# Performance work log

Hardware: AMD Instinct MI355X
Metric: run time of the kernel (lower is better)

The kernel has to match this reference:

```python
import jax, jax.numpy as jnp
import numpy as np

BN_EPS = 1e-3  # keras BatchNormalization default epsilon
B, T, D, V = 2048, 100, 64, 200000
N_OTHER, V_OTHER, D_OTHER = 2, 10000, 32
DNN = (256, 128, 64)


def _gru(seq_x, Wx, Wh, b, valid, att=None):
    """GRU / AUGRU scan. seq_x [B,T,D]; valid [B,T] bool; att [B,T] or None.
    AUGRU: update gate z is scaled by the attention score a_t;
    invalid (padded) steps hold the previous state (dynamic length)."""
    Bs, Ts, _ = seq_x.shape
    H = Wh.shape[0]
    xproj = jnp.einsum('btd,dh->bth', seq_x, Wx) + b          # [B,T,3H]
    xproj = jnp.transpose(xproj, (1, 0, 2))                    # [T,B,3H]
    v = jnp.transpose(valid, (1, 0))[:, :, None]               # [T,B,1]
    if att is None:
        a = jnp.ones((Ts, Bs, 1), seq_x.dtype)
    else:
        a = jnp.transpose(att, (1, 0))[:, :, None]
    h0 = jnp.zeros((Bs, H), seq_x.dtype)

    def step(h, inp):
        xp, vi, ai = inp
        xz, xr, xh = jnp.split(xp, 3, -1)
        hz, hr, hh = jnp.split(h @ Wh, 3, -1)
        z = jax.nn.sigmoid(xz + hz) * ai
        r = jax.nn.sigmoid(xr + hr)
        cand = jnp.tanh(xh + r * hh)
        hn = (1.0 - z) * h + z * cand
        hn = jnp.where(vi, hn, h)
        return hn, hn

    final, seq = jax.lax.scan(step, h0, (xproj, v, a))
    return final, jnp.transpose(seq, (1, 0, 2))                # [B,T,H]


def _dice(x, alpha):
    # Dice activation, inference-mode BN (moving mean 0, var 1)
    p = jax.nn.sigmoid(x * (1.0 / np.sqrt(1.0 + BN_EPS)))
    return p * x + (1.0 - p) * alpha * x


def _attention(q, keys, mask, W1, b1, W2, b2, W3, b3):
    # DIN-style attention: MLP over [q, k, q-k, q*k], masked softmax over time
    qe = jnp.broadcast_to(q[:, None, :], keys.shape)
    info = jnp.concatenate([qe, keys, qe - keys, qe * keys], -1)   # [B,T,4D]
    h = jax.nn.sigmoid(info @ W1 + b1)
    h = jax.nn.sigmoid(h @ W2 + b2)
    logits = (h @ W3 + b3)[..., 0]                                  # [B,T]
    logits = jnp.where(mask, logits, jnp.float32(-1e9))
    return jax.nn.softmax(logits, axis=-1)


def setup_inputs() -> dict:
    key = jax.random.key(0)
    ks = jax.random.split(key, 32)
    s = 0.05
    inp = {
        'dense_inputs': jax.random.normal(ks[0], (B, 8), jnp.float32),
        'sparse_inputs': jax.random.randint(ks[1], (B, N_OTHER), 0, V_OTHER, jnp.int32),
        'seq_inputs': jax.random.randint(ks[2], (B, T, 1), 0, V, jnp.int32),
        'no_click_seq': jax.random.randint(ks[3], (B, T, 1), 0, V, jnp.int32),
        'item_inputs': jax.random.randint(ks[4], (B, 1), 0, V, jnp.int32),
        'hist_real_len': jax.random.randint(ks[5], (B,), 1, T + 1, jnp.int32),
        'emb_item': jax.random.normal(ks[6], (V, D), jnp.float32) * s,
        'emb_neg': jax.random.normal(ks[7], (V, D), jnp.float32) * s,
        'emb_other': jax.random.normal(ks[8], (N_OTHER, V_OTHER, D_OTHER), jnp.float32) * s,
        'gru1_Wx': jax.random.normal(ks[9], (D, 3 * D), jnp.float32) * s,
        'gru1_Wh': jax.random.normal(ks[10], (D, 3 * D), jnp.float32) * s,
        'gru1_b': jnp.zeros((3 * D,), jnp.float32),
        'att_W1': jax.random.normal(ks[11], (4 * D, 64), jnp.float32) * s,
        'att_b1': jnp.zeros((64,), jnp.float32),
        'att_W2': jax.random.normal(ks[12], (64, 16), jnp.float32) * s,
        'att_b2': jnp.zeros((16,), jnp.float32),
        'att_W3': jax.random.normal(ks[13], (16, 1), jnp.float32) * s,
        'att_b3': jnp.zeros((1,), jnp.float32),
        'gru2_Wx': jax.random.normal(ks[14], (D, 3 * D), jnp.float32) * s,
        'gru2_Wh': jax.random.normal(ks[15], (D, 3 * D), jnp.float32) * s,
        'gru2_b': jnp.zeros((3 * D,), jnp.float32),
    }
    in_dim = D + D + 8 + N_OTHER * D_OTHER  # final_state + target + other_info
    inp['bn_gamma'] = jnp.ones((in_dim,), jnp.float32)
    inp['bn_beta'] = jnp.zeros((in_dim,), jnp.float32)
    dims = (in_dim,) + DNN
    for i in range(3):
        inp[f'ffn_W{i}'] = jax.random.normal(ks[16 + i], (dims[i], dims[i + 1]), jnp.float32) * s
        inp[f'ffn_b{i}'] = jnp.zeros((dims[i + 1],), jnp.float32)
        inp[f'dice_a{i}'] = jnp.full((dims[i + 1],), 0.25, jnp.float32)
    inp['out_W'] = jax.random.normal(ks[20], (DNN[-1], 1), jnp.float32) * s
    inp['out_b'] = jnp.zeros((1,), jnp.float32)
    return inp


def reference(dense_inputs, sparse_inputs, seq_inputs, no_click_seq, item_inputs,
              hist_real_len, emb_item, emb_neg, emb_other, gru1_Wx, gru1_Wh, gru1_b,
              att_W1, att_b1, att_W2, att_b2, att_W3, att_b3, gru2_Wx, gru2_Wh, gru2_b,
              bn_gamma, bn_beta, ffn_W0, ffn_b0, dice_a0, ffn_W1, ffn_b1, dice_a1,
              ffn_W2, ffn_b2, dice_a2, out_W, out_b):
    # other (non-behavior) info: dense feats ++ other sparse embeddings
    other = jnp.concatenate(
        [dense_inputs] + [emb_other[i][sparse_inputs[:, i]] for i in range(N_OTHER)], -1)
    seq_embed = emb_item[seq_inputs[:, :, 0]]          # [B,T,D]
    neg_embed = emb_neg[no_click_seq[:, :, 0]]         # [B,T,D]
    target = emb_item[item_inputs[:, 0]]               # [B,D]
    mask = seq_inputs[:, :, 0] != 0                    # [B,T]
    valid = jnp.arange(T)[None, :] < hist_real_len[:, None]

    # interest extraction: plain GRU over behavior sequence
    _, seq_h = _gru(seq_embed, gru1_Wx, gru1_Wh, gru1_b, valid)

    # auxiliary loss: h_t should predict the next clicked item vs a negative
    m = mask[:, 1:].astype(seq_h.dtype)
    h = seq_h[:, :-1]
    p_pos = jax.nn.sigmoid(jnp.sum(h * seq_embed[:, 1:], -1))
    p_neg = jax.nn.sigmoid(jnp.sum(h * neg_embed[:, 1:], -1))
    aux_loss = -jnp.sum(m * (jnp.log(p_pos + 1e-8) + jnp.log(1.0 - p_neg + 1e-8))) / (jnp.sum(m) + 1e-8)

    # interest evolution: attention-gated AUGRU
    scores = _attention(target, seq_h, mask, att_W1, att_b1, att_W2, att_b2, att_W3, att_b3)
    final_state, _ = _gru(seq_h, gru2_Wx, gru2_Wh, gru2_b, valid, att=scores)

    x = jnp.concatenate([final_state, target, other], -1)
    x = bn_gamma * x * (1.0 / np.sqrt(1.0 + BN_EPS)) + bn_beta   # inference BN
    x = _dice(x @ ffn_W0 + ffn_b0, dice_a0)
    x = _dice(x @ ffn_W1 + ffn_b1, dice_a1)
    x = _dice(x @ ffn_W2 + ffn_b2, dice_a2)
    out = jax.nn.sigmoid(x @ out_W + out_b)                       # [B,1]
    return out, aux_loss
```

## Files before the change

kernel.cpp:

```cpp
#include <hip/hip_runtime.h>
#include <math.h>


#define DEV __device__ __forceinline__

constexpr int BB = 2048;
constexpr int TT = 100;

typedef __attribute__((ext_vector_type(8))) short bf16x8;
typedef __attribute__((ext_vector_type(4))) float f32x4;

#define MFMA16(a, b, c) __builtin_amdgcn_mfma_f32_16x16x32_bf16(a, b, c, 0, 0, 0)

DEV float sigmoidf_(float x) { return 1.0f / (1.0f + __expf(-x)); }
DEV float tanhf_(float x)    { return 1.0f - 2.0f / (__expf(2.0f * x) + 1.0f); }
DEV short f2bf(float f) {
    unsigned u = __float_as_uint(f);
    u = (u + 0x7FFFu + ((u >> 16) & 1u)) >> 16;
    return (short)u;
}
DEV float bf2f(short s) { return __uint_as_float(((unsigned)(unsigned short)s) << 16); }

DEV void sync_lds() {
    __builtin_amdgcn_sched_barrier(0);
    asm volatile("s_waitcnt lgkmcnt(0)\n\ts_barrier" ::: "memory");
    __builtin_amdgcn_sched_barrier(0);
}

__global__ void k_prep(const float* __restrict__ W1, float* Wq, float* Wk, float* Wp, float* aux_acc) {
    int i = blockIdx.x * 256 + threadIdx.x;
    if (i < 4096) {
        int k = i >> 6, c = i & 63;
        float a  = W1[k * 64 + c];
        float bb = W1[(64 + k) * 64 + c];
        float cc = W1[(128 + k) * 64 + c];
        float dd = W1[(192 + k) * 64 + c];
        Wq[i] = a + cc;
        Wk[i] = bb - cc;
        Wp[i] = dd;
    }
    if (blockIdx.x == 0 && threadIdx.x == 0) { aux_acc[0] = 0.0f; aux_acc[1] = 0.0f; }
}

__global__ __launch_bounds__(256)
void k_prepW(const float* __restrict__ Wa, const float* __restrict__ Wb,
             const float* __restrict__ Wc, const float* __restrict__ Wd,
             short* __restrict__ oa, short* __restrict__ ob,
             short* __restrict__ oc, short* __restrict__ od) {
    const float* W; short* o;
    switch (blockIdx.y) {
        case 0:  W = Wa; o = oa; break;
        case 1:  W = Wb; o = ob; break;
        case 2:  W = Wc; o = oc; break;
        default: W = Wd; o = od; break;
    }
    int d = blockIdx.x * 256 + threadIdx.x;
    int frag = d >> 9, l = (d >> 3) & 63, i = d & 7;
    int n = frag >> 1, kt = frag & 1;
    int k = kt * 32 + ((l >> 4) << 3) + i;
    int c = (n << 4) + (l & 15);
    o[d] = f2bf(W[k * 192 + c]);
}

__global__ __launch_bounds__(256)
void k_prepA(const float* __restrict__ Wk, const float* __restrict__ Wp,
             short* __restrict__ oK, short* __restrict__ oP) {
    int d = blockIdx.x * 256 + threadIdx.x;
    int mat = d >> 12, i = d & 4095;
    int f = i >> 9, l = (i >> 3) & 63, e = i & 7;
    int kt = f >> 2, n = f & 3;
    int k = kt * 32 + ((l >> 4) << 3) + e;
    int c = (n << 4) + (l & 15);
    if (mat == 0) oK[i] = f2bf(Wk[k * 64 + c]);
    else          oP[i] = f2bf(Wp[k * 64 + c]);
}

__global__ __launch_bounds__(64)
void k_target(const int* __restrict__ item, const float* __restrict__ emb_item,
              const float* __restrict__ Wq, const float* __restrict__ b1,
              float* target, float* qproj) {
    int b = blockIdx.x, c = threadIdx.x;
    __shared__ float q[64];
    int idx = item[b];
    float tv = emb_item[(size_t)idx * 64 + c];
    target[b * 64 + c] = tv;
    q[c] = tv;
    __syncthreads();
    float acc = b1[c];
#pragma unroll
    for (int k = 0; k < 64; ++k) acc = fmaf(q[k], Wq[k * 64 + c], acc);
    qproj[b * 64 + c] = acc;
}

template <int MODE>
__global__ __launch_bounds__(256, 2)
void k_scan(const int* __restrict__ seq_idx, const float* __restrict__ embf,
            const short* __restrict__ seqb,
            const short* __restrict__ WxB, const short* __restrict__ WhB,
            const float* __restrict__ bias, const int* __restrict__ hist_len,
            const float* __restrict__ scores,
            short* __restrict__ seq_out, float* __restrict__ final_out) {
    __shared__ short hA[2][1024];

    const int tid  = threadIdx.x;
    const int w    = tid >> 6;
    const int lane = tid & 63;
    const int lr   = lane & 15;
    const int kg   = lane >> 4;
    const int b0   = blockIdx.x * 4;

    for (int i = tid; i < 2048; i += 256) ((short*)hA)[i] = 0;

    bf16x8 bx[3][2], bh[3][2];
#pragma unroll
    for (int n3 = 0; n3 < 3; ++n3) {
        int n = w + n3 * 4;
#pragma unroll
        for (int kt = 0; kt < 2; ++kt) {
            bx[n3][kt] = *(const bf16x8*)(WxB + (((n * 2 + kt) * 64 + lane) << 3));
            bh[n3][kt] = *(const bf16x8*)(WhB + (((n * 2 + kt) * 64 + lane) << 3));
        }
    }

    const int   c0  = (w << 4) + lr;
    const float bz  = bias[c0];
    const float brr = bias[64 + c0];
    const float bhb = bias[128 + c0];
    const bool  act = (kg == 0);

    int   hist[4];
    float h[4] = {0.f, 0.f, 0.f, 0.f};
#pragma unroll
    for (int j = 0; j < 4; ++j) hist[j] = hist_len[b0 + j];

    const int rload = (lr < 4) ? lr : 3;
    bf16x8 ecb0, ecb1;
    float  scc[4] = {1.f, 1.f, 1.f, 1.f};

    {
        if (MODE == 0) {
            int idx = seq_idx[(b0 + rload) * TT];
            const float* eb = embf + (size_t)idx * 64;
            float4 f0 = *(const float4*)(eb + kg * 8);
            float4 f1 = *(const float4*)(eb + kg * 8 + 4);
            float4 f2 = *(const float4*)(eb + 32 + kg * 8);
            float4 f3 = *(const float4*)(eb + 32 + kg * 8 + 4);
            ecb0[0] = f2bf(f0.x); ecb0[1] = f2bf(f0.y); ecb0[2] = f2bf(f0.z); ecb0[3] = f2bf(f0.w);
            ecb0[4] = f2bf(f1.x); ecb0[5] = f2bf(f1.y); ecb0[6] = f2bf(f1.z); ecb0[7] = f2bf(f1.w);
            ecb1[0] = f2bf(f2.x); ecb1[1] = f2bf(f2.y); ecb1[2] = f2bf(f2.z); ecb1[3] = f2bf(f2.w);
            ecb1[4] = f2bf(f3.x); ecb1[5] = f2bf(f3.y); ecb1[6] = f2bf(f3.z); ecb1[7] = f2bf(f3.w);
        } else {
            const short* eb = seqb + ((size_t)(b0 + rload) * TT) * 64;
            ecb0 = *(const bf16x8*)(eb + kg * 8);
            ecb1 = *(const bf16x8*)(eb + 32 + kg * 8);
        }
        if (MODE == 1) {
#pragma unroll
            for (int j = 0; j < 4; ++j) scc[j] = scores[(b0 + j) * TT];
        }
    }
    __syncthreads();

    const int so0 = lr * 64 + (((kg    ) ^ (lr & 7)) << 3);
    const int so1 = lr * 64 + (((4 + kg) ^ (lr & 7)) << 3);

    for (int t = 0; t < TT; ++t) {
        const int buf = t & 1;
        bf16x8 ha0 = *(const bf16x8*)&hA[buf][so0];
        bf16x8 ha1 = *(const bf16x8*)&hA[buf][so1];

        float4 f0, f1, f2, f3;
        bf16x8 nb0, nb1;
        float scn[4];
        const bool haven = (t < TT - 1);
        if (haven) {
            if (MODE == 0) {
                int idx = seq_idx[(b0 + rload) * TT + t + 1];
                const float* eb = embf + (size_t)idx * 64;
                f0 = *(const float4*)(eb + kg * 8);
                f1 = *(const float4*)(eb + kg * 8 + 4);
                f2 = *(const float4*)(eb + 32 + kg * 8);
                f3 = *(const float4*)(eb + 32 + kg * 8 + 4);
            } else {
                const short* eb = seqb + ((size_t)(b0 + rload) * TT + (t + 1)) * 64;
                nb0 = *(const bf16x8*)(eb + kg * 8);
                nb1 = *(const bf16x8*)(eb + 32 + kg * 8);
#pragma unroll
                for (int j = 0; j < 4; ++j) scn[j] = scores[(b0 + j) * TT + t + 1];
            }
        }

        f32x4 az  = {0.f, 0.f, 0.f, 0.f};
        f32x4 ar  = {0.f, 0.f, 0.f, 0.f};
        f32x4 ahx = {0.f, 0.f, 0.f, 0.f};
        f32x4 ahh = {0.f, 0.f, 0.f, 0.f};
        az  = MFMA16(ecb0, bx[0][0], az);  az  = MFMA16(ecb1, bx[0][1], az);
        az  = MFMA16(ha0,  bh[0][0], az);  az  = MFMA16(ha1,  bh[0][1], az);
        ar  = MFMA16(ecb0, bx[1][0], ar);  ar  = MFMA16(ecb1, bx[1][1], ar);
        ar  = MFMA16(ha0,  bh[1][0], ar);  ar  = MFMA16(ha1,  bh[1][1], ar);
        ahx = MFMA16(ecb0, bx[2][0], ahx); ahx = MFMA16(ecb1, bx[2][1], ahx);
        ahh = MFMA16(ha0,  bh[2][0], ahh); ahh = MFMA16(ha1,  bh[2][1], ahh);

        if (act) {
#pragma unroll
            for (int j = 0; j < 4; ++j) {
                float a01  = (MODE == 1) ? scc[j] : 1.0f;
                float z    = sigmoidf_(az[j] + bz) * a01;
                float r    = sigmoidf_(ar[j] + brr);
                float cand = tanhf_(ahx[j] + bhb + r * ahh[j]);
                float hn   = h[j] + z * (cand - h[j]);
                h[j] = (t < hist[j]) ? hn : h[j];
                short v = f2bf(h[j]);
                int sw = j * 64 + (((c0 >> 3) ^ j) << 3) + (c0 & 7);
                hA[buf ^ 1][sw] = v;
                if (MODE == 0)
                    seq_out[((size_t)(b0 + j) * TT + t) * 64 + c0] = v;
            }
        }

        if (haven) {
            if (MODE == 0) {
                ecb0[0] = f2bf(f0.x); ecb0[1] = f2bf(f0.y); ecb0[2] = f2bf(f0.z); ecb0[3] = f2bf(f0.w);
                ecb0[4] = f2bf(f1.x); ecb0[5] = f2bf(f1.y); ecb0[6] = f2bf(f1.z); ecb0[7] = f2bf(f1.w);
                ecb1[0] = f2bf(f2.x); ecb1[1] = f2bf(f2.y); ecb1[2] = f2bf(f2.z); ecb1[3] = f2bf(f2.w);
                ecb1[4] = f2bf(f3.x); ecb1[5] = f2bf(f3.y); ecb1[6] = f2bf(f3.z); ecb1[7] = f2bf(f3.w);
            } else {
                ecb0 = nb0; ecb1 = nb1;
#pragma unroll
                for (int j = 0; j < 4; ++j) scc[j] = scn[j];
            }
        }
        sync_lds();
    }

    if (MODE == 1 && act) {
#pragma unroll
        for (int j = 0; j < 4; ++j)
            final_out[(b0 + j) * 64 + c0] = h[j];
    }
}

__global__ __launch_bounds__(256)
void k_attn(const short* __restrict__ seq_h, const float* __restrict__ target,
            const float* __restrict__ qproj, const int* __restrict__ seq_idx,
            const short* __restrict__ WkB, const short* __restrict__ WpB,
            const float* __restrict__ W2g, const float* __restrict__ b2g,
            const float* __restrict__ W3g, const float* __restrict__ b3g,
            float* __restrict__ scores) {
    __shared__ __align__(16) short keysb[7168];
    __shared__ __align__(16) short pkb[7168];
    __shared__ float W2_s[1024];
    __shared__ float q_s[64], qp_s[64];
    __shared__ float b2_s[16], W3_s[16];
    __shared__ float lg[112];

    const int b = blockIdx.x, tid = threadIdx.x;
    const int w = tid >> 6, lane = tid & 63;

    bf16x8 BK[2][4], BP[2][4];
#pragma unroll
    for (int kt = 0; kt < 2; ++kt)
#pragma unroll
        for (int n = 0; n < 4; ++n) {
            BK[kt][n] = *(const bf16x8*)(WkB + (((kt * 4 + n) * 64 + lane) << 3));
            BP[kt][n] = *(const bf16x8*)(WpB + (((kt * 4 + n) * 64 + lane) << 3));
        }
    if (tid < 64)  { q_s[tid] = target[b * 64 + tid]; qp_s[tid] = qproj[b * 64 + tid]; }
    if (tid >= 64 && tid < 80) { b2_s[tid - 64] = b2g[tid - 64]; W3_s[tid - 64] = W3g[tid - 64]; }
    for (int i = tid; i < 1024; i += 256) W2_s[i] = W2g[i];
    __syncthreads();

    for (int i4 = tid; i4 < 1792; i4 += 256) {
        int r = i4 >> 4, c4 = i4 & 15;
        short4 kv, pv;
        if (r < TT) {
            short4 sv = *(const short4*)(seq_h + (size_t)b * (TT * 64) + r * 64 + c4 * 4);
            float q0 = q_s[c4 * 4], q1 = q_s[c4 * 4 + 1], q2 = q_s[c4 * 4 + 2], q3 = q_s[c4 * 4 + 3];
            kv = sv;
            pv = make_short4(f2bf(bf2f(sv.x) * q0), f2bf(bf2f(sv.y) * q1),
                             f2bf(bf2f(sv.z) * q2), f2bf(bf2f(sv.w) * q3));
        } else {
            kv = make_short4(0, 0, 0, 0); pv = kv;
        }
        int off = r * 128 + ((c4 * 8) ^ ((r & 7) << 4));
        *(short4*)((char*)keysb + off) = kv;
        *(short4*)((char*)pkb + off)   = pv;
    }
    __syncthreads();

    for (int rt = w; rt < 7; rt += 4) {
        const int r0 = rt * 16;
        const int arow = r0 + (lane & 15);
        const int kb = lane >> 4;
        bf16x8 AK[2], AP[2];
#pragma unroll
        for (int kt = 0; kt < 2; ++kt) {
            int off = arow * 128 + (((kt * 64) + kb * 16) ^ ((arow & 7) << 4));
            AK[kt] = *(const bf16x8*)((const char*)keysb + off);
            AP[kt] = *(const bf16x8*)((const char*)pkb + off);
        }
        f32x4 C[4];
#pragma unroll
        for (int n = 0; n < 4; ++n) { C[n] = (f32x4){0.f, 0.f, 0.f, 0.f}; }
#pragma unroll
        for (int n = 0; n < 4; ++n) {
            C[n] = MFMA16(AK[0], BK[0][n], C[n]);
            C[n] = MFMA16(AK[1], BK[1][n], C[n]);
            C[n] = MFMA16(AP[0], BP[0][n], C[n]);
            C[n] = MFMA16(AP[1], BP[1][n], C[n]);
        }
#pragma unroll
        for (int n = 0; n < 4; ++n) {
            int col = n * 16 + (lane & 15);
            float qp = qp_s[col];
#pragma unroll
            for (int j = 0; j < 4; ++j) {
                int row = r0 + (lane >> 4) * 4 + j;
                float h1 = sigmoidf_(C[n][j] + qp);
                int off = row * 128 + ((col * 2) ^ ((row & 7) << 4));
                *(short*)((char*)pkb + off) = f2bf(h1);
            }
        }
    }
    __syncthreads();

    {
        int t = tid >> 1, half = tid & 1;
        if (t < TT) {
            int j0 = half * 8;
            float acc[8];
#pragma unroll
            for (int jj = 0; jj < 8; ++jj) acc[jj] = b2_s[j0 + jj];
#pragma unroll
            for (int ch = 0; ch < 8; ++ch) {
                int off = t * 128 + ((ch * 16) ^ ((t & 7) << 4));
                bf16x8 hv = *(const bf16x8*)((const char*)pkb + off);
#pragma unroll
                for (int e = 0; e < 8; ++e) {
                    float hf = bf2f(hv[e]);
                    int k = ch * 8 + e;
#pragma unroll
                    for (int jj = 0; jj < 8; ++jj)
                        acc[jj] = fmaf(hf, W2_s[k * 16 + j0 + jj], acc[jj]);
                }
            }
            float part = 0.f;
#pragma unroll
            for (int jj = 0; jj < 8; ++jj) part += sigmoidf_(acc[jj]) * W3_s[j0 + jj];
            part += __shfl_xor(part, 1);
            if (half == 0) {
                bool m = (seq_idx[b * TT + t] != 0);
                lg[t] = m ? (part + b3g[0]) : -1e9f;
            }
        }
    }
    __syncthreads();

    if (w == 0) {
        float a  = lg[lane];
        float bv = (lane + 64 < TT) ? lg[lane + 64] : -1e30f;
        float mx = fmaxf(a, bv);
#pragma unroll
        for (int s = 32; s; s >>= 1) mx = fmaxf(mx, __shfl_xor(mx, s));
        float ea = __expf(a - mx);
        float eb = (lane + 64 < TT) ? __expf(bv - mx) : 0.f;
        float sum = ea + eb;
#pragma unroll
        for (int s = 32; s; s >>= 1) sum += __shfl_xor(sum, s);
        float inv = 1.0f / sum;
        scores[b * TT + lane] = ea * inv;
        if (lane + 64 < TT) scores[b * TT + lane + 64] = eb * inv;
    }
}

__global__ __launch_bounds__(256)
void k_aux(const short* __restrict__ seq_h, const int* __restrict__ seq_idx,
           const int* __restrict__ neg_idx, const float* __restrict__ emb_item,
           const float* __restrict__ emb_neg, float* aux_acc) {
    int b = blockIdx.x, tid = threadIdx.x;
    int w = tid >> 6, l = tid & 63;
    __shared__ float pnum[4], pden[4];
    float num = 0.0f, den = 0.0f;
    for (int i = 0; i < 25; ++i) {
        int t = w + i * 4;
        if (t >= TT - 1) break;
        int ip  = seq_idx[b * TT + t + 1];
        int in_ = neg_idx[b * TT + t + 1];
        float h = bf2f(seq_h[(size_t)b * (TT * 64) + t * 64 + l]);
        float dp = h * emb_item[(size_t)ip * 64 + l];
        float dn = h * emb_neg[(size_t)in_ * 64 + l];
#pragma unroll
        for (int s = 32; s; s >>= 1) { dp += __shfl_xor(dp, s); dn += __shfl_xor(dn, s); }
        if (l == 0 && ip != 0) {
            float pp = sigmoidf_(dp), pn = sigmoidf_(dn);
            num += __logf(pp + 1e-8f) + __logf(1.0f - pn + 1e-8f);
            den += 1.0f;
        }
    }
    if (l == 0) { pnum[w] = num; pden[w] = den; }
    __syncthreads();
    if (tid == 0) {
        atomicAdd(&aux_acc[0], pnum[0] + pnum[1] + pnum[2] + pnum[3]);
        atomicAdd(&aux_acc[1], pden[0] + pden[1] + pden[2] + pden[3]);
    }
}

__global__ __launch_bounds__(256)
void k_mlp(const float* __restrict__ final_state, const float* __restrict__ target,
           const float* __restrict__ dense, const int* __restrict__ sparse,
           const float* __restrict__ emb_other,
           const float* __restrict__ bng, const float* __restrict__ bnb,
           const float* __restrict__ W0, const float* __restrict__ bb0, const float* __restrict__ al0,
           const float* __restrict__ W1, const float* __restrict__ bb1, const float* __restrict__ al1,
           const float* __restrict__ W2, const float* __restrict__ bb2, const float* __restrict__ al2,
           const float* __restrict__ Wo, const float* __restrict__ bo,
           const float* __restrict__ aux_acc, float* __restrict__ out) {
    const float inv1 = 0.9995003747f;
    int tid = threadIdx.x, b0 = blockIdx.x * 8;
    __shared__ float x_s[8][200], h1_s[8][256], h2_s[8][128], h3_s[8][64];

    for (int i = tid; i < 8 * 200; i += 256) {
        int r = i / 200, cc = i - r * 200, b = b0 + r;
        float v;
        if (cc < 64)       v = final_state[b * 64 + cc];
        else if (cc < 128) v = target[b * 64 + cc - 64];
        else if (cc < 136) v = dense[b * 8 + cc - 128];
        else if (cc < 168) v = emb_other[(size_t)sparse[b * 2 + 0] * 32 + (cc - 136)];
        else               v = emb_other[(size_t)10000 * 32 + (size_t)sparse[b * 2 + 1] * 32 + (cc - 168)];
        x_s[r][cc] = fmaf(bng[cc] * inv1, v, bnb[cc]);
    }
    __syncthreads();
    {
        int r = tid >> 5, cb = tid & 31;
        float acc[8];
#pragma unroll
        for (int j = 0; j < 8; ++j) acc[j] = bb0[cb + 32 * j];
        for (int k = 0; k < 200; ++k) {
            float xv = x_s[r][k];
#pragma unroll
            for (int j = 0; j < 8; ++j) acc[j] = fmaf(xv, W0[k * 256 + cb + 32 * j], acc[j]);
        }
#pragma unroll
        for (int j = 0; j < 8; ++j) {
            float y = acc[j];
            float p = sigmoidf_(y * inv1);
            h1_s[r][cb + 32 * j] = y * (p + (1.0f - p) * al0[cb + 32 * j]);
        }
    }
    __syncthreads();
    {
        int r = tid >> 5, cb = tid & 31;
        float acc[4];
#pragma unroll
        for (int j = 0; j < 4; ++j) acc[j] = bb1[cb + 32 * j];
        for (int k = 0; k < 256; ++k) {
            float xv = h1_s[r][k];
#pragma unroll
            for (int j = 0; j < 4; ++j) acc[j] = fmaf(xv, W1[k * 128 + cb + 32 * j], acc[j]);
        }
#pragma unroll
        for (int j = 0; j < 4; ++j) {
            float y = acc[j];
            float p = sigmoidf_(y * inv1);
            h2_s[r][cb + 32 * j] = y * (p + (1.0f - p) * al1[cb + 32 * j]);
        }
    }
    __syncthreads();
    {
        int r = tid >> 5, cb = tid & 31;
        float acc[2] = {bb2[cb], bb2[cb + 32]};
        for (int k = 0; k < 128; ++k) {
            float xv = h2_s[r][k];
            acc[0] = fmaf(xv, W2[k * 64 + cb], acc[0]);
            acc[1] = fmaf(xv, W2[k * 64 + cb + 32], acc[1]);
        }
#pragma unroll
        for (int j = 0; j < 2; ++j) {
            float y = acc[j];
            float p = sigmoidf_(y * inv1);
            h3_s[r][cb + 32 * j] = y * (p + (1.0f - p) * al2[cb + 32 * j]);
        }
    }
    __syncthreads();
    {
        int r = tid >> 5, l = tid & 31;
        float v = h3_s[r][l] * Wo[l] + h3_s[r][l + 32] * Wo[l + 32];
#pragma unroll
        for (int s = 16; s; s >>= 1) v += __shfl_xor(v, s, 32);
        if (l == 0) out[b0 + r] = sigmoidf_(v + bo[0]);
    }
    if (blockIdx.x == 0 && tid == 0) {
        out[BB] = -aux_acc[0] / (aux_acc[1] + 1e-8f);
    }
}

extern "C" void kernel_launch(void* const* d_in, const int* in_sizes, int n_in,
                              void* d_out, int out_size, void* d_ws, size_t ws_size,
                              hipStream_t stream) {
    (void)in_sizes; (void)n_in; (void)out_size; (void)ws_size;
    const float* dense    = (const float*)d_in[0];
    const int*   sparse   = (const int*)d_in[1];
    const int*   seq_in   = (const int*)d_in[2];
    const int*   neg_in   = (const int*)d_in[3];
    const int*   item_in  = (const int*)d_in[4];
    const int*   hist     = (const int*)d_in[5];
    const float* emb_item = (const float*)d_in[6];
    const float* emb_neg  = (const float*)d_in[7];
    const float* emb_oth  = (const float*)d_in[8];
    const float* g1Wx = (const float*)d_in[9];
    const float* g1Wh = (const float*)d_in[10];
    const float* g1b  = (const float*)d_in[11];
    const float* aW1  = (const float*)d_in[12];
    const float* ab1  = (const float*)d_in[13];
    const float* aW2  = (const float*)d_in[14];
    const float* ab2  = (const float*)d_in[15];
    const float* aW3  = (const float*)d_in[16];
    const float* ab3  = (const float*)d_in[17];
    const float* g2Wx = (const float*)d_in[18];
    const float* g2Wh = (const float*)d_in[19];
    const float* g2b  = (const float*)d_in[20];
    const float* bng  = (const float*)d_in[21];
    const float* bnb  = (const float*)d_in[22];
    const float* W0   = (const float*)d_in[23];
    const float* b0f  = (const float*)d_in[24];
    const float* a0f  = (const float*)d_in[25];
    const float* W1f  = (const float*)d_in[26];
    const float* b1f  = (const float*)d_in[27];
    const float* a1f  = (const float*)d_in[28];
    const float* W2f  = (const float*)d_in[29];
    const float* b2f  = (const float*)d_in[30];
    const float* a2f  = (const float*)d_in[31];
    const float* Wo   = (const float*)d_in[32];
    const float* bo   = (const float*)d_in[33];

    float* ws          = (float*)d_ws;
    short* seq_hb      = (short*)ws;
    float* scoresW     = ws + 6553600;
    float* target      = scoresW + 204800;
    float* qproj       = target + 131072;
    float* final_state = qproj + 131072;
    float* Wq          = final_state + 131072;
    float* Wk          = Wq + 4096;
    float* Wp          = Wk + 4096;
    short* WxB1        = (short*)(Wp + 4096);
    short* WhB1        = WxB1 + 12288;
    short* WxB2        = WhB1 + 12288;
    short* WhB2        = WxB2 + 12288;
    short* WkB         = WhB2 + 12288;
    short* WpB         = WkB + 4096;
    float* aux_acc     = (float*)(WpB + 4096);

    k_prep<<<16, 256, 0, stream>>>(aW1, Wq, Wk, Wp, aux_acc);
    k_prepW<<<dim3(48, 4), 256, 0, stream>>>(g1Wx, g1Wh, g2Wx, g2Wh, WxB1, WhB1, WxB2, WhB2);
    k_prepA<<<32, 256, 0, stream>>>(Wk, Wp, WkB, WpB);
    k_target<<<BB, 64, 0, stream>>>(item_in, emb_item, Wq, ab1, target, qproj);
    k_scan<0><<<512, 256, 0, stream>>>(seq_in, emb_item, nullptr, WxB1, WhB1, g1b, hist,
                                       nullptr, seq_hb, nullptr);
    k_attn<<<BB, 256, 0, stream>>>(seq_hb, target, qproj, seq_in, WkB, WpB, aW2, ab2, aW3, ab3, scoresW);
    k_scan<1><<<512, 256, 0, stream>>>(seq_in, nullptr, seq_hb, WxB2, WhB2, g2b, hist,
                                       scoresW, nullptr, final_state);
    k_aux<<<BB, 256, 0, stream>>>(seq_hb, seq_in, neg_in, emb_item, emb_neg, aux_acc);
    k_mlp<<<256, 256, 0, stream>>>(final_state, target, dense, sparse, emb_oth, bng, bnb,
                                   W0, b0f, a0f, W1f, b1f, a1f, W2f, b2f, a2f, Wo, bo,
                                   aux_acc, (float*)d_out);
}
```

Measured before the change: 598.2 us.

## Fill all 16 MFMA rows per scan block and pre-gather embeddings to bf16

Each GRU scan block now processes 16 batch rows instead of 4, so the 16-row MFMA tiles and the gate epilogue are fully used rather than three-quarters idle. This drops the scan grid from 512 to 128 blocks. The embedding lookup and fp32-to-bf16 conversion for the first GRU move into a separate gather kernel that writes a bf16 sequence buffer, which takes the dependent gather off the sequential step loop. In exchange it adds an extra pass over global memory and workspace, and with only 128 blocks many CUs sit idle during the latency-bound scan.

New measurement: 519.1 us. 1.15x faster.

```diff
diff --git a/kernel.cpp b/kernel.cpp
--- a/kernel.cpp
+++ b/kernel.cpp
@@ -92,10 +92,27 @@
     qproj[b * 64 + c] = acc;
 }
 
+__global__ __launch_bounds__(256)
+void k_gather(const int* __restrict__ seq_idx, const float* __restrict__ emb,
+              short* __restrict__ out) {
+    int g = blockIdx.x * 256 + threadIdx.x;
+    int row = g >> 2, q = g & 3;
+    int idx = seq_idx[row];
+    const float4* src = (const float4*)(emb + (size_t)idx * 64 + q * 16);
+    float4 f0 = src[0], f1 = src[1], f2 = src[2], f3 = src[3];
+    bf16x8 o0, o1;
+    o0[0] = f2bf(f0.x); o0[1] = f2bf(f0.y); o0[2] = f2bf(f0.z); o0[3] = f2bf(f0.w);
+    o0[4] = f2bf(f1.x); o0[5] = f2bf(f1.y); o0[6] = f2bf(f1.z); o0[7] = f2bf(f1.w);
+    o1[0] = f2bf(f2.x); o1[1] = f2bf(f2.y); o1[2] = f2bf(f2.z); o1[3] = f2bf(f2.w);
+    o1[4] = f2bf(f3.x); o1[5] = f2bf(f3.y); o1[6] = f2bf(f3.z); o1[7] = f2bf(f3.w);
+    short* dst = out + (size_t)row * 64 + q * 16;
+    *(bf16x8*)dst = o0;
+    *(bf16x8*)(dst + 8) = o1;
+}
+
 template <int MODE>
-__global__ __launch_bounds__(256, 2)
-void k_scan(const int* __restrict__ seq_idx, const float* __restrict__ embf,
-            const short* __restrict__ seqb,
+__global__ __launch_bounds__(256)
+void k_scan(const short* __restrict__ esrc,
             const short* __restrict__ WxB, const short* __restrict__ WhB,
             const float* __restrict__ bias, const int* __restrict__ hist_len,
             const float* __restrict__ scores,
@@ -107,7 +124,7 @@
     const int lane = tid & 63;
     const int lr   = lane & 15;
     const int kg   = lane >> 4;
-    const int b0   = blockIdx.x * 4;
+    const int b0   = blockIdx.x * 16;
 
     for (int i = tid; i < 2048; i += 256) ((short*)hA)[i] = 0;
 
@@ -126,38 +143,19 @@
     const float bz  = bias[c0];
     const float brr = bias[64 + c0];
     const float bhb = bias[128 + c0];
-    const bool  act = (kg == 0);
 
     int   hist[4];
     float h[4] = {0.f, 0.f, 0.f, 0.f};
 #pragma unroll
-    for (int j = 0; j < 4; ++j) hist[j] = hist_len[b0 + j];
-
-    const int rload = (lr < 4) ? lr : 3;
-    bf16x8 ecb0, ecb1;
-    float  scc[4] = {1.f, 1.f, 1.f, 1.f};
-
-    {
-        if (MODE == 0) {
-            int idx = seq_idx[(b0 + rload) * TT];
-            const float* eb = embf + (size_t)idx * 64;
-            float4 f0 = *(const float4*)(eb + kg * 8);
-            float4 f1 = *(const float4*)(eb + kg * 8 + 4);
-            float4 f2 = *(const float4*)(eb + 32 + kg * 8);
-            float4 f3 = *(const float4*)(eb + 32 + kg * 8 + 4);
-            ecb0[0] = f2bf(f0.x); ecb0[1] = f2bf(f0.y); ecb0[2] = f2bf(f0.z); ecb0[3] = f2bf(f0.w);
-            ecb0[4] = f2bf(f1.x); ecb0[5] = f2bf(f1.y); ecb0[6] = f2bf(f1.z); ecb0[7] = f2bf(f1.w);
-            ecb1[0] = f2bf(f2.x); ecb1[1] = f2bf(f2.y); ecb1[2] = f2bf(f2.z); ecb1[3] = f2bf(f2.w);
-            ecb1[4] = f2bf(f3.x); ecb1[5] = f2bf(f3.y); ecb1[6] = f2bf(f3.z); ecb1[7] = f2bf(f3.w);
-        } else {
-            const short* eb = seqb + ((size_t)(b0 + rload) * TT) * 64;
-            ecb0 = *(const bf16x8*)(eb + kg * 8);
-            ecb1 = *(const bf16x8*)(eb + 32 + kg * 8);
-        }
-        if (MODE == 1) {
-#pragma unroll
-            for (int j = 0; j < 4; ++j) scc[j] = scores[(b0 + j) * TT];
-        }
+    for (int j = 0; j < 4; ++j) hist[j] = hist_len[b0 + kg * 4 + j];
+
+    const size_t erow = (size_t)(b0 + lr) * TT * 64;
+    bf16x8 e0 = *(const bf16x8*)(esrc + erow + kg * 8);
+    bf16x8 e1 = *(const bf16x8*)(esrc + erow + 32 + kg * 8);
+    float scc[4] = {1.f, 1.f, 1.f, 1.f};
+    if (MODE == 1) {
+#pragma unroll
+        for (int j = 0; j < 4; ++j) scc[j] = scores[(b0 + kg * 4 + j) * TT];
     }
     __syncthreads();
 
@@ -169,24 +167,15 @@
         bf16x8 ha0 = *(const bf16x8*)&hA[buf][so0];
         bf16x8 ha1 = *(const bf16x8*)&hA[buf][so1];
 
-        float4 f0, f1, f2, f3;
-        bf16x8 nb0, nb1;
+        bf16x8 n0, n1;
         float scn[4];
         const bool haven = (t < TT - 1);
         if (haven) {
-            if (MODE == 0) {
-                int idx = seq_idx[(b0 + rload) * TT + t + 1];
-                const float* eb = embf + (size_t)idx * 64;
-                f0 = *(const float4*)(eb + kg * 8);
-                f1 = *(const float4*)(eb + kg * 8 + 4);
-                f2 = *(const float4*)(eb + 32 + kg * 8);
-                f3 = *(const float4*)(eb + 32 + kg * 8 + 4);
-            } else {
-                const short* eb = seqb + ((size_t)(b0 + rload) * TT + (t + 1)) * 64;
-                nb0 = *(const bf16x8*)(eb + kg * 8);
-                nb1 = *(const bf16x8*)(eb + 32 + kg * 8);
-#pragma unroll
-                for (int j = 0; j < 4; ++j) scn[j] = scores[(b0 + j) * TT + t + 1];
+            n0 = *(const bf16x8*)(esrc + erow + (size_t)(t + 1) * 64 + kg * 8);
+            n1 = *(const bf16x8*)(esrc + erow + (size_t)(t + 1) * 64 + 32 + kg * 8);
+            if (MODE == 1) {
+#pragma unroll
+                for (int j = 0; j < 4; ++j) scn[j] = scores[(b0 + kg * 4 + j) * TT + t + 1];
             }
         }
 
@@ -194,38 +183,31 @@
         f32x4 ar  = {0.f, 0.f, 0.f, 0.f};
         f32x4 ahx = {0.f, 0.f, 0.f, 0.f};
         f32x4 ahh = {0.f, 0.f, 0.f, 0.f};
-        az  = MFMA16(ecb0, bx[0][0], az);  az  = MFMA16(ecb1, bx[0][1], az);
-        az  = MFMA16(ha0,  bh[0][0], az);  az  = MFMA16(ha1,  bh[0][1], az);
-        ar  = MFMA16(ecb0, bx[1][0], ar);  ar  = MFMA16(ecb1, bx[1][1], ar);
-        ar  = MFMA16(ha0,  bh[1][0], ar);  ar  = MFMA16(ha1,  bh[1][1], ar);
-        ahx = MFMA16(ecb0, bx[2][0], ahx); ahx = MFMA16(ecb1, bx[2][1], ahx);
-        ahh = MFMA16(ha0,  bh[2][0], ahh); ahh = MFMA16(ha1,  bh[2][1], ahh);
-
-        if (act) {
-#pragma unroll
-            for (int j = 0; j < 4; ++j) {
-                float a01  = (MODE == 1) ? scc[j] : 1.0f;
-                float z    = sigmoidf_(az[j] + bz) * a01;
-                float r    = sigmoidf_(ar[j] + brr);
-                float cand = tanhf_(ahx[j] + bhb + r * ahh[j]);
-                float hn   = h[j] + z * (cand - h[j]);
-                h[j] = (t < hist[j]) ? hn : h[j];
-                short v = f2bf(h[j]);
-                int sw = j * 64 + (((c0 >> 3) ^ j) << 3) + (c0 & 7);
-                hA[buf ^ 1][sw] = v;
-                if (MODE == 0)
-                    seq_out[((size_t)(b0 + j) * TT + t) * 64 + c0] = v;
-            }
+        az  = MFMA16(e0,  bx[0][0], az);  az  = MFMA16(e1,  bx[0][1], az);
+        az  = MFMA16(ha0, bh[0][0], az);  az  = MFMA16(ha1, bh[0][1], az);
+        ar  = MFMA16(e0,  bx[1][0], ar);  ar  = MFMA16(e1,  bx[1][1], ar);
+        ar  = MFMA16(ha0, bh[1][0], ar);  ar  = MFMA16(ha1, bh[1][1], ar);
+        ahx = MFMA16(e0,  bx[2][0], ahx); ahx = MFMA16(e1,  bx[2][1], ahx);
+        ahh = MFMA16(ha0, bh[2][0], ahh); ahh = MFMA16(ha1, bh[2][1], ahh);
+
+#pragma unroll
+        for (int j = 0; j < 4; ++j) {
+            int rr = kg * 4 + j;
+            float a01  = (MODE == 1) ? scc[j] : 1.0f;
+            float z    = sigmoidf_(az[j] + bz) * a01;
+            float r    = sigmoidf_(ar[j] + brr);
+            float cand = tanhf_(ahx[j] + bhb + r * ahh[j]);
+            float hn   = h[j] + z * (cand - h[j]);
+            h[j] = (t < hist[j]) ? hn : h[j];
+            short v = f2bf(h[j]);
+            hA[buf ^ 1][rr * 64 + ((((c0 >> 3)) ^ (rr & 7)) << 3) + (c0 & 7)] = v;
+            if (MODE == 0)
+                seq_out[((size_t)(b0 + rr) * TT + t) * 64 + c0] = v;
         }
 
         if (haven) {
-            if (MODE == 0) {
-                ecb0[0] = f2bf(f0.x); ecb0[1] = f2bf(f0.y); ecb0[2] = f2bf(f0.z); ecb0[3] = f2bf(f0.w);
-                ecb0[4] = f2bf(f1.x); ecb0[5] = f2bf(f1.y); ecb0[6] = f2bf(f1.z); ecb0[7] = f2bf(f1.w);
-                ecb1[0] = f2bf(f2.x); ecb1[1] = f2bf(f2.y); ecb1[2] = f2bf(f2.z); ecb1[3] = f2bf(f2.w);
-                ecb1[4] = f2bf(f3.x); ecb1[5] = f2bf(f3.y); ecb1[6] = f2bf(f3.z); ecb1[7] = f2bf(f3.w);
-            } else {
-                ecb0 = nb0; ecb1 = nb1;
+            e0 = n0; e1 = n1;
+            if (MODE == 1) {
 #pragma unroll
                 for (int j = 0; j < 4; ++j) scc[j] = scn[j];
             }
@@ -233,10 +215,10 @@
         sync_lds();
     }
 
-    if (MODE == 1 && act) {
+    if (MODE == 1) {
 #pragma unroll
         for (int j = 0; j < 4; ++j)
-            final_out[(b0 + j) * 64 + c0] = h[j];
+            final_out[(b0 + kg * 4 + j) * 64 + c0] = h[j];
     }
 }
 
@@ -535,7 +517,8 @@
 
     float* ws          = (float*)d_ws;
     short* seq_hb      = (short*)ws;
-    float* scoresW     = ws + 6553600;
+    short* e1b         = (short*)(ws + 6553600);
+    float* scoresW     = ws + 13107200;
     float* target      = scoresW + 204800;
     float* qproj       = target + 131072;
     float* final_state = qproj + 131072;
@@ -554,11 +537,10 @@
     k_prepW<<<dim3(48, 4), 256, 0, stream>>>(g1Wx, g1Wh, g2Wx, g2Wh, WxB1, WhB1, WxB2, WhB2);
     k_prepA<<<32, 256, 0, stream>>>(Wk, Wp, WkB, WpB);
     k_target<<<BB, 64, 0, stream>>>(item_in, emb_item, Wq, ab1, target, qproj);
-    k_scan<0><<<512, 256, 0, stream>>>(seq_in, emb_item, nullptr, WxB1, WhB1, g1b, hist,
-                                       nullptr, seq_hb, nullptr);
+    k_gather<<<3200, 256, 0, stream>>>(seq_in, emb_item, e1b);
+    k_scan<0><<<128, 256, 0, stream>>>(e1b, WxB1, WhB1, g1b, hist, nullptr, seq_hb, nullptr);
     k_attn<<<BB, 256, 0, stream>>>(seq_hb, target, qproj, seq_in, WkB, WpB, aW2, ab2, aW3, ab3, scoresW);
-    k_scan<1><<<512, 256, 0, stream>>>(seq_in, nullptr, seq_hb, WxB2, WhB2, g2b, hist,
-                                       scoresW, nullptr, final_state);
+    k_scan<1><<<128, 256, 0, stream>>>(seq_hb, WxB2, WhB2, g2b, hist, scoresW, nullptr, final_state);
     k_aux<<<BB, 256, 0, stream>>>(seq_hb, seq_in, neg_in, emb_item, emb_neg, aux_acc);
     k_mlp<<<256, 256, 0, stream>>>(final_state, target, dense, sparse, emb_oth, bng, bnb,
                                    W0, b0f, a0f, W1f, b1f, a1f, W2f, b2f, a2f, Wo, bo,
```
